# Performance work log

Measured on AMD Instinct MI355X. Metric: run time of the kernel, lower is better.

Reference implementation:

```python
import math
import jax, jax.numpy as jnp
import numpy as np

TOP_K = 2
N_EXP = 8
EVAL_CAPACITY_FACTOR = 2.0
MIN_CAPACITY = 4


def setup_inputs() -> dict:
    key = jax.random.key(0)
    k1, k2 = jax.random.split(key)
    x = jax.random.normal(k1, (2, 2048, 1024), dtype=jnp.float32)
    # nn.Linear(n_embd, n_experts, bias=False) weight: [n_exp, n_embd]
    w_g = jax.random.normal(k2, (N_EXP, 1024), dtype=jnp.float32) * 0.02
    return {"x": x, "w_g": w_g}


def reference(x, w_g):
    B, T, H = x.shape
    N = B * T                      # num_tokens
    E = w_g.shape[0]               # n_experts
    K = TOP_K
    capacity = max(int(math.floor(K * EVAL_CAPACITY_FACTOR * N / E)), MIN_CAPACITY)

    x_flat = x.reshape(N, H)
    logits = x_flat @ w_g.T                      # [N, E]

    top_k_logits, top_k_idx = jax.lax.top_k(logits, K)   # [N, K]

    # scatter top-k logits into a -inf canvas, then softmax over experts
    router_probs = jnp.full_like(logits, -jnp.inf)
    router_probs = router_probs.at[jnp.arange(N)[:, None], top_k_idx].set(top_k_logits)
    router_probs = jax.nn.softmax(router_probs, axis=-1)  # [N, E]

    # capacity-based dispatch
    exp_mask = jax.nn.one_hot(top_k_idx, E, dtype=jnp.int32)   # [N, K, E]
    exp_mask = jnp.transpose(exp_mask, (1, 0, 2))              # [K, N, E]

    exp_rank = jnp.cumsum(exp_mask.reshape(K * N, E), axis=0) - 1
    exp_rank = exp_rank.reshape(K, N, E)                       # position within expert

    exp_mask = exp_mask * (exp_rank < capacity).astype(jnp.int32)
    used_capacity = jnp.sum(exp_mask, axis=(0, 1))             # [E]

    exp_rank_tok = jnp.sum(exp_mask * exp_rank, axis=-1)       # [K, N]

    exp_weights = exp_mask.astype(router_probs.dtype) * router_probs[None]  # [K, N, E]
    exp_rank_sc = jax.nn.one_hot(exp_rank_tok, capacity, dtype=router_probs.dtype)  # [K, N, C]

    cb_weight = jnp.einsum('kne,knc->nec', exp_weights, exp_rank_sc)  # [N, E, C]
    sec_mask = cb_weight.astype(bool)
    return used_capacity, cb_weight, sec_mask
```

## Files before the change

kernel.cpp:

```cpp
#include <hip/hip_runtime.h>
#include <math.h>


#define HDIM 1024
#define NEXP 8

__global__ __launch_bounds__(256) void logits_topk_kernel(
    const float* __restrict__ x, const float* __restrict__ wg,
    int* __restrict__ expert_slot, float* __restrict__ prob_slot, int N) {
  __shared__ float w_lds[NEXP * HDIM];
  const int tid = threadIdx.x;
  for (int i = tid; i < NEXP * HDIM / 4; i += blockDim.x)
    ((float4*)w_lds)[i] = ((const float4*)wg)[i];
  __syncthreads();

  const int wave = tid >> 6;
  const int lane = tid & 63;
  const int n = blockIdx.x * 4 + wave;
  if (n >= N) return;

  const float* xr = x + (size_t)n * HDIM;
  float acc[NEXP];
#pragma unroll
  for (int e = 0; e < NEXP; e++) acc[e] = 0.0f;

#pragma unroll
  for (int j = 0; j < HDIM; j += 256) {
    float4 xv = ((const float4*)(xr + j))[lane];
#pragma unroll
    for (int e = 0; e < NEXP; e++) {
      float4 wv = ((const float4*)(w_lds + e * HDIM + j))[lane];
      acc[e] += xv.x * wv.x + xv.y * wv.y + xv.z * wv.z + xv.w * wv.w;
    }
  }

#pragma unroll
  for (int e = 0; e < NEXP; e++) {
    float v = acc[e];
    for (int off = 32; off > 0; off >>= 1) v += __shfl_down(v, off, 64);
    acc[e] = v;
  }

  if (lane == 0) {
    int b0 = 0;
    float v0 = acc[0];
#pragma unroll
    for (int e = 1; e < NEXP; e++) {
      if (acc[e] > v0) { v0 = acc[e]; b0 = e; }
    }
    int b1 = -1;
    float v1 = -INFINITY;
#pragma unroll
    for (int e = 0; e < NEXP; e++) {
      if (e == b0) continue;
      if (acc[e] > v1) { v1 = acc[e]; b1 = e; }
    }
    float e2 = expf(v1 - v0);
    float p0 = 1.0f / (1.0f + e2);
    float p1 = e2 / (1.0f + e2);
    expert_slot[n] = b0;
    expert_slot[N + n] = b1;
    prob_slot[n] = p0;
    prob_slot[N + n] = p1;
  }
}

__global__ __launch_bounds__(256) void count_kernel(
    const int* __restrict__ expert_slot, int* __restrict__ counts, int S) {
  const int gid = blockIdx.x * 256 + threadIdx.x;
  const int wave = gid >> 6;
  const int lane = gid & 63;
  const int s = wave * 64 + lane;
  if (s >= S) return;
  const int e = expert_slot[s];
#pragma unroll
  for (int w = 0; w < NEXP; w++) {
    unsigned long long m = __ballot(e == w);
    if (lane == w) counts[wave * NEXP + w] = __popcll(m);
  }
}

__global__ __launch_bounds__(512) void scan_kernel(
    const int* __restrict__ counts, int* __restrict__ base,
    float* __restrict__ used_cap, int nchunk, int C) {
  const int w = threadIdx.x >> 6;
  const int lane = threadIdx.x & 63;

  int v0 = (lane < nchunk) ? counts[lane * NEXP + w] : 0;
  int s0 = v0;
  for (int off = 1; off < 64; off <<= 1) {
    int t = __shfl_up(s0, off, 64);
    if (lane >= off) s0 += t;
  }
  int total0 = __shfl(s0, 63, 64);
  if (lane < nchunk) base[lane * NEXP + w] = s0 - v0;

  int i1 = 64 + lane;
  int v1 = (i1 < nchunk) ? counts[i1 * NEXP + w] : 0;
  int s1 = v1;
  for (int off = 1; off < 64; off <<= 1) {
    int t = __shfl_up(s1, off, 64);
    if (lane >= off) s1 += t;
  }
  if (i1 < nchunk) base[i1 * NEXP + w] = total0 + s1 - v1;
  int total = total0 + __shfl(s1, 63, 64);
  if (lane == 0) used_cap[w] = (float)(total < C ? total : C);
}

__global__ __launch_bounds__(256) void scatter_kernel(
    const int* __restrict__ expert_slot, const float* __restrict__ prob_slot,
    const int* __restrict__ base, float* __restrict__ cb,
    float* __restrict__ sec, int N, int C) {
  const int gid = blockIdx.x * 256 + threadIdx.x;
  const int wave = gid >> 6;
  const int lane = gid & 63;
  const int s = wave * 64 + lane;
  if (s >= 2 * N) return;
  const int e = expert_slot[s];
  const float p = prob_slot[s];
  const unsigned long long below = (1ull << lane) - 1ull;
  int rank = -1;
#pragma unroll
  for (int w = 0; w < NEXP; w++) {
    unsigned long long m = __ballot(e == w);
    if (e == w) rank = base[wave * NEXP + w] + __popcll(m & below);
  }
  if (rank < C) {
    int n = (s >= N) ? (s - N) : s;
    size_t off = ((size_t)n * NEXP + e) * (size_t)C + (size_t)rank;
    cb[off] = p;
    sec[off] = (p != 0.0f) ? 1.0f : 0.0f;
  }
}

extern "C" void kernel_launch(void* const* d_in, const int* in_sizes, int n_in,
                              void* d_out, int out_size, void* d_ws, size_t ws_size,
                              hipStream_t stream) {
  const float* x = (const float*)d_in[0];
  const float* wg = (const float*)d_in[1];

  const int N = in_sizes[0] / HDIM;
  const int K = 2;
  int capacity = (int)floor((double)K * 2.0 * (double)N / (double)NEXP);
  if (capacity < 4) capacity = 4;

  const int S = 2 * N;
  const int nchunk = (S + 63) / 64;

  float* out = (float*)d_out;
  float* used_cap = out;
  float* cb = out + NEXP;
  float* sec = cb + (size_t)N * NEXP * (size_t)capacity;

  char* ws = (char*)d_ws;
  int* expert_slot = (int*)ws;
  float* prob_slot = (float*)(ws + 4 * (size_t)S);
  int* counts = (int*)(ws + 8 * (size_t)S);
  int* base = (int*)(ws + 8 * (size_t)S + 4 * (size_t)(nchunk * NEXP));

  hipMemsetAsync(d_out, 0, sizeof(float) * (size_t)out_size, stream);

  logits_topk_kernel<<<(N + 3) / 4, 256, 0, stream>>>(x, wg, expert_slot,
                                                      prob_slot, N);
  count_kernel<<<(S + 255) / 256, 256, 0, stream>>>(expert_slot, counts, S);
  scan_kernel<<<1, 512, 0, stream>>>(counts, base, used_cap, nchunk, capacity);
  scatter_kernel<<<(S + 255) / 256, 256, 0, stream>>>(expert_slot, prob_slot,
                                                      base, cb, sec, N,
                                                      capacity);
}
```

Before: 532.8 us.

## Fuse count/scan/rank into one block and write outputs densely without memset

Merges the count, scan and rank phases into a single 1024-thread block that keeps per-chunk counts and bases in LDS. It also drops the full-output memset and instead writes every cb/sec element once, one block per token with float4 stores, placing the probability at the routed rank. This removes one pass over a large output buffer and two kernel launches. In exchange the rank phase is serialized on one workgroup, and the indexing assumes capacity is a power of two and divisible by 4.

Measured after the change: 568.5 us. 6.7% more time.

```diff
diff --git a/kernel.cpp b/kernel.cpp
--- a/kernel.cpp
+++ b/kernel.cpp
@@ -65,71 +65,104 @@
   }
 }
 
-__global__ __launch_bounds__(256) void count_kernel(
-    const int* __restrict__ expert_slot, int* __restrict__ counts, int S) {
-  const int gid = blockIdx.x * 256 + threadIdx.x;
-  const int wave = gid >> 6;
-  const int lane = gid & 63;
-  const int s = wave * 64 + lane;
-  if (s >= S) return;
-  const int e = expert_slot[s];
+#define MAXCHUNK 128
+__global__ __launch_bounds__(1024) void rank_kernel(
+    const int* __restrict__ expert_slot, int* __restrict__ rank_slot,
+    float* __restrict__ used_cap, int S, int C) {
+  __shared__ int cnt[MAXCHUNK * 9];
+  __shared__ int base[MAXCHUNK * 9];
+  const int tid = threadIdx.x;
+  const int wave = tid >> 6;
+  const int lane = tid & 63;
+  const int nchunk = (S + 63) >> 6;
+
+  for (int c = wave; c < nchunk; c += 16) {
+    const int s = c * 64 + lane;
+    const int e = (s < S) ? expert_slot[s] : -1;
 #pragma unroll
-  for (int w = 0; w < NEXP; w++) {
-    unsigned long long m = __ballot(e == w);
-    if (lane == w) counts[wave * NEXP + w] = __popcll(m);
+    for (int w = 0; w < NEXP; w++) {
+      unsigned long long m = __ballot(e == w);
+      if (lane == w) cnt[c * 9 + w] = __popcll(m);
+    }
+  }
+  __syncthreads();
+
+  if (wave < NEXP) {
+    const int w = wave;
+    int v0 = (lane < nchunk) ? cnt[lane * 9 + w] : 0;
+    int s0 = v0;
+    for (int off = 1; off < 64; off <<= 1) {
+      int t = __shfl_up(s0, off, 64);
+      if (lane >= off) s0 += t;
+    }
+    int total0 = __shfl(s0, 63, 64);
+    if (lane < nchunk) base[lane * 9 + w] = s0 - v0;
+
+    const int i1 = 64 + lane;
+    int v1 = (i1 < nchunk) ? cnt[i1 * 9 + w] : 0;
+    int s1 = v1;
+    for (int off = 1; off < 64; off <<= 1) {
+      int t = __shfl_up(s1, off, 64);
+      if (lane >= off) s1 += t;
+    }
+    if (i1 < nchunk) base[i1 * 9 + w] = total0 + s1 - v1;
+    int total = total0 + __shfl(s1, 63, 64);
+    if (lane == 0) used_cap[w] = (float)(total < C ? total : C);
+  }
+  __syncthreads();
+
+  for (int c = wave; c < nchunk; c += 16) {
+    const int s = c * 64 + lane;
+    const int e = (s < S) ? expert_slot[s] : -1;
+    const unsigned long long below = (1ull << lane) - 1ull;
+    int rank = -1;
+#pragma unroll
+    for (int w = 0; w < NEXP; w++) {
+      unsigned long long m = __ballot(e == w);
+      if (e == w) rank = base[c * 9 + w] + __popcll(m & below);
+    }
+    if (s < S) rank_slot[s] = rank;
   }
 }
 
-__global__ __launch_bounds__(512) void scan_kernel(
-    const int* __restrict__ counts, int* __restrict__ base,
-    float* __restrict__ used_cap, int nchunk, int C) {
-  const int w = threadIdx.x >> 6;
-  const int lane = threadIdx.x & 63;
+__global__ __launch_bounds__(256) void write_all_kernel(
+    const int* __restrict__ expert_slot, const float* __restrict__ prob_slot,
+    const int* __restrict__ rank_slot, float* __restrict__ cb,
+    float* __restrict__ sec, int N, int C) {
+  const int n = blockIdx.x;
+  __shared__ int rk[NEXP];
+  __shared__ float pp[NEXP];
+  if (threadIdx.x == 0) {
+#pragma unroll
+    for (int e = 0; e < NEXP; e++) { rk[e] = -1; pp[e] = 0.0f; }
+    const int e0 = expert_slot[n];
+    const int r0 = rank_slot[n];
+    if (r0 < C) { rk[e0] = r0; pp[e0] = prob_slot[n]; }
+    const int e1 = expert_slot[N + n];
+    const int r1 = rank_slot[N + n];
+    if (r1 < C) { rk[e1] = r1; pp[e1] = prob_slot[N + n]; }
+  }
+  __syncthreads();
 
-  int v0 = (lane < nchunk) ? counts[lane * NEXP + w] : 0;
-  int s0 = v0;
-  for (int off = 1; off < 64; off <<= 1) {
-    int t = __shfl_up(s0, off, 64);
-    if (lane >= off) s0 += t;
-  }
-  int total0 = __shfl(s0, 63, 64);
-  if (lane < nchunk) base[lane * NEXP + w] = s0 - v0;
-
-  int i1 = 64 + lane;
-  int v1 = (i1 < nchunk) ? counts[i1 * NEXP + w] : 0;
-  int s1 = v1;
-  for (int off = 1; off < 64; off <<= 1) {
-    int t = __shfl_up(s1, off, 64);
-    if (lane >= off) s1 += t;
-  }
-  if (i1 < nchunk) base[i1 * NEXP + w] = total0 + s1 - v1;
-  int total = total0 + __shfl(s1, 63, 64);
-  if (lane == 0) used_cap[w] = (float)(total < C ? total : C);
-}
-
-__global__ __launch_bounds__(256) void scatter_kernel(
-    const int* __restrict__ expert_slot, const float* __restrict__ prob_slot,
-    const int* __restrict__ base, float* __restrict__ cb,
-    float* __restrict__ sec, int N, int C) {
-  const int gid = blockIdx.x * 256 + threadIdx.x;
-  const int wave = gid >> 6;
-  const int lane = gid & 63;
-  const int s = wave * 64 + lane;
-  if (s >= 2 * N) return;
-  const int e = expert_slot[s];
-  const float p = prob_slot[s];
-  const unsigned long long below = (1ull << lane) - 1ull;
-  int rank = -1;
-#pragma unroll
-  for (int w = 0; w < NEXP; w++) {
-    unsigned long long m = __ballot(e == w);
-    if (e == w) rank = base[wave * NEXP + w] + __popcll(m & below);
-  }
-  if (rank < C) {
-    int n = (s >= N) ? (s - N) : s;
-    size_t off = ((size_t)n * NEXP + e) * (size_t)C + (size_t)rank;
-    cb[off] = p;
-    sec[off] = (p != 0.0f) ? 1.0f : 0.0f;
+  const int span4 = (NEXP * C) >> 2;
+  float4* cbp = (float4*)(cb + (size_t)n * NEXP * C);
+  float4* secp = (float4*)(sec + (size_t)n * NEXP * C);
+  const int cshift = 31 - __builtin_clz(C);
+  for (int i = threadIdx.x; i < span4; i += 256) {
+    const int f = i << 2;
+    const int e = f >> cshift;
+    const int idx = f & (C - 1);
+    const int rank = rk[e];
+    float4 v = {0.0f, 0.0f, 0.0f, 0.0f};
+    float4 m = {0.0f, 0.0f, 0.0f, 0.0f};
+    const int d = rank - idx;
+    if (d >= 0 && d < 4) {
+      const float p = pp[e];
+      ((float*)&v)[d] = p;
+      ((float*)&m)[d] = (p != 0.0f) ? 1.0f : 0.0f;
+    }
+    cbp[i] = v;
+    secp[i] = m;
   }
 }
 
@@ -145,7 +178,6 @@
   if (capacity < 4) capacity = 4;
 
   const int S = 2 * N;
-  const int nchunk = (S + 63) / 64;
 
   float* out = (float*)d_out;
   float* used_cap = out;
@@ -155,16 +187,12 @@
   char* ws = (char*)d_ws;
   int* expert_slot = (int*)ws;
   float* prob_slot = (float*)(ws + 4 * (size_t)S);
-  int* counts = (int*)(ws + 8 * (size_t)S);
-  int* base = (int*)(ws + 8 * (size_t)S + 4 * (size_t)(nchunk * NEXP));
-
-  hipMemsetAsync(d_out, 0, sizeof(float) * (size_t)out_size, stream);
+  int* rank_slot = (int*)(ws + 8 * (size_t)S);
 
   logits_topk_kernel<<<(N + 3) / 4, 256, 0, stream>>>(x, wg, expert_slot,
                                                       prob_slot, N);
-  count_kernel<<<(S + 255) / 256, 256, 0, stream>>>(expert_slot, counts, S);
-  scan_kernel<<<1, 512, 0, stream>>>(counts, base, used_cap, nchunk, capacity);
-  scatter_kernel<<<(S + 255) / 256, 256, 0, stream>>>(expert_slot, prob_slot,
-                                                      base, cb, sec, N,
-                                                      capacity);
+  rank_kernel<<<1, 1024, 0, stream>>>(expert_slot, rank_slot, used_cap, S,
+                                      capacity);
+  write_all_kernel<<<N, 256, 0, stream>>>(expert_slot, prob_slot, rank_slot,
+                                          cb, sec, N, capacity);
 }
```
